# Kernel tuning notes

Hardware: AMD Instinct MI355X
Metric: run time of the kernel (lower is better)

The kernel has to match this reference:

```python
import jax, jax.numpy as jnp
import numpy as np

B, L, DM, H = 2, 4096, 1024, 16
D = DM // H


def setup_inputs() -> dict:
    key = jax.random.key(0)
    ks = jax.random.split(key, 11)
    s = 1.0 / np.sqrt(DM)
    return {
        "query": jax.random.normal(ks[0], (B, L, DM), jnp.float32),
        "key": jax.random.normal(ks[1], (B, L, DM), jnp.float32),
        "value": jax.random.normal(ks[2], (B, L, DM), jnp.float32),
        "Wq": jax.random.normal(ks[3], (DM, DM), jnp.float32) * s,
        "bq": jnp.zeros((DM,), jnp.float32),
        "Wk": jax.random.normal(ks[4], (DM, DM), jnp.float32) * s,
        "bk": jnp.zeros((DM,), jnp.float32),
        "Wv": jax.random.normal(ks[5], (DM, DM), jnp.float32) * s,
        "bv": jnp.zeros((DM,), jnp.float32),
        "Wo": jax.random.normal(ks[6], (DM, DM), jnp.float32) * s,
        "bo": jnp.zeros((DM,), jnp.float32),
    }


def _split_heads(x):
    # (B, L, DM) -> (B, H, L, D)
    b, l, _ = x.shape
    return x.reshape(b, l, H, D).transpose(0, 2, 1, 3)


def reference(query, key, value, Wq, bq, Wk, bk, Wv, bv, Wo, bo):
    q = _split_heads(query @ Wq + bq)
    k = _split_heads(key @ Wk + bk)
    v = _split_heads(value @ Wv + bv)
    # ELU+1 feature map
    q = jax.nn.elu(q) + 1.0
    k = jax.nn.elu(k) + 1.0
    # Original: kv = einsum('bhld,bhmd->bhlm', k, v); out = einsum('bhlm,bhld->bhmd', kv, q)
    # Equivalent (associativity): out[m,d] = sum_e v[m,e] * (sum_l k[l,e] q[l,d])
    S = jnp.einsum('bhle,bhld->bhed', k, q)          # (B,H,D,D)
    out = jnp.einsum('bhme,bhed->bhmd', v, S)        # (B,H,L,D)
    denom = jnp.einsum('bhld,bhld->bhl', q, k) + 1e-6
    out = out / denom[..., None]
    # combine heads: (B,H,L,D) -> (B,L,DM)
    out = out.transpose(0, 2, 1, 3).reshape(out.shape[0], -1, DM)
    # out_dense; dropout is identity at inference
    return out @ Wo + bo
```

## Files before the change

kernel.cpp:

```cpp
#include <hip/hip_runtime.h>

#define B_  2
#define L_  4096
#define DM_ 1024
#define H_  16
#define D_  64
#define M_  (B_ * L_)

typedef unsigned short u16;
typedef short bf16x8 __attribute__((ext_vector_type(8)));
typedef float f32x4  __attribute__((ext_vector_type(4)));

typedef const __attribute__((address_space(1))) void* as1_cvp;
typedef __attribute__((address_space(3))) void* as3_vp;

__device__ __forceinline__ float b2f(u16 u) {
    union { unsigned int i; float f; } x; x.i = ((unsigned int)u) << 16; return x.f;
}
__device__ __forceinline__ u16 f2b(float f) {
    unsigned int x = __float_as_uint(f);
    return (u16)((x + 0x7fffu + ((x >> 16) & 1u)) >> 16);
}

__global__ void prep_kernel(
    const float* __restrict__ query, const float* __restrict__ key, const float* __restrict__ value,
    u16* __restrict__ qb, u16* __restrict__ kb, u16* __restrict__ vb,
    const float* __restrict__ w0, const float* __restrict__ w1,
    const float* __restrict__ w2, const float* __restrict__ w3,
    u16* __restrict__ t0, u16* __restrict__ t1, u16* __restrict__ t2, u16* __restrict__ t3)
{
    __shared__ float tile[32][33];
    const int bx = blockIdx.x;
    const int t  = threadIdx.x;
    if (bx < 24576) {
        int z = bx >> 13;
        int i = (bx & 8191) * 256 + t;
        const float* in = z == 0 ? query : (z == 1 ? key : value);
        u16* out        = z == 0 ? qb    : (z == 1 ? kb  : vb);
        float4 v = ((const float4*)in)[i];
        ushort4 o;
        o.x = f2b(v.x); o.y = f2b(v.y); o.z = f2b(v.z); o.w = f2b(v.w);
        ((ushort4*)out)[i] = o;
    } else {
        int bz = bx - 24576;
        int z  = bz >> 10;
        int rem = bz & 1023;
        int gx = rem & 31, gy = rem >> 5;
        const float* W = z == 0 ? w0 : z == 1 ? w1 : z == 2 ? w2 : w3;
        u16* Wt        = z == 0 ? t0 : z == 1 ? t1 : z == 2 ? t2 : t3;
        int tx = t & 31, ty = t >> 5;
        int n  = gx * 32 + tx;
        int k0 = gy * 32;
#pragma unroll
        for (int i = 0; i < 4; ++i)
            tile[ty + i * 8][tx] = W[(size_t)(k0 + ty + i * 8) * DM_ + n];
        __syncthreads();
#pragma unroll
        for (int i = 0; i < 4; ++i) {
            int nn = gx * 32 + ty + i * 8;
            Wt[(size_t)nn * DM_ + k0 + tx] = f2b(tile[tx][ty + i * 8]);
        }
    }
}

__global__ __launch_bounds__(256, 4) void gemm_qkv_kernel(
    const u16* __restrict__ qb, const u16* __restrict__ kb, const u16* __restrict__ vb,
    const u16* __restrict__ Wqt, const u16* __restrict__ Wkt, const u16* __restrict__ Wvt,
    const float* __restrict__ bq, const float* __restrict__ bk, const float* __restrict__ bv,
    u16* __restrict__ QpT, u16* __restrict__ KpT, u16* __restrict__ Vp)
{
    const int z = blockIdx.z;
    const u16* A    = z == 0 ? qb  : z == 1 ? kb  : vb;
    const u16* Bt   = z == 0 ? Wqt : z == 1 ? Wkt : Wvt;
    const float* bias = z == 0 ? bq : z == 1 ? bk : bv;

    __shared__ __align__(16) u16 smem[16384];
    u16* As = smem;
    u16* Bs = smem + 8192;

    const int t    = threadIdx.x;
    const int lane = t & 63;
    const int wave = t >> 6;
    const int wr   = wave >> 1;
    const int wc   = wave & 1;
    const int quad = lane >> 4;
    const int l16  = lane & 15;
    const int m0   = blockIdx.x * 128;
    const int n0   = blockIdx.y * 128;
    const int K    = DM_;

    f32x4 acc[4][4] = {};

    for (int kt = 0; kt < K; kt += 64) {
#pragma unroll
        for (int i = 0; i < 4; ++i) {
            int c   = i * 256 + t;
            int row = c >> 3;
            int kc  = c & 7;
            int cbase = i * 256 + wave * 64;
            const u16* gA = A  + (size_t)(m0 + row) * K + kt + kc * 8;
            const u16* gB = Bt + (size_t)(n0 + row) * K + kt + kc * 8;
            __builtin_amdgcn_global_load_lds((as1_cvp)gA, (as3_vp)(As + cbase * 8), 16, 0, 0);
            __builtin_amdgcn_global_load_lds((as1_cvp)gB, (as3_vp)(Bs + cbase * 8), 16, 0, 0);
        }
        __syncthreads();
#pragma unroll
        for (int ks = 0; ks < 2; ++ks) {
            bf16x8 af[4], bfr[4];
#pragma unroll
            for (int it = 0; it < 4; ++it)
                af[it] = *(const bf16x8*)(As + (wr * 64 + it * 16 + l16) * 64 + ks * 32 + quad * 8);
#pragma unroll
            for (int jt = 0; jt < 4; ++jt)
                bfr[jt] = *(const bf16x8*)(Bs + (wc * 64 + jt * 16 + l16) * 64 + ks * 32 + quad * 8);
#pragma unroll
            for (int it = 0; it < 4; ++it)
#pragma unroll
                for (int jt = 0; jt < 4; ++jt)
                    acc[it][jt] = __builtin_amdgcn_mfma_f32_16x16x32_bf16(
                        af[it], bfr[jt], acc[it][jt], 0, 0, 0);
        }
        __syncthreads();
    }

    if (z == 2) {
#pragma unroll
        for (int it = 0; it < 4; ++it) {
            int row0 = m0 + wr * 64 + it * 16 + quad * 4;
#pragma unroll
            for (int jt = 0; jt < 4; ++jt) {
                int col = n0 + wc * 64 + jt * 16 + l16;
                float bv2 = bias[col];
#pragma unroll
                for (int r = 0; r < 4; ++r)
                    Vp[(size_t)(row0 + r) * DM_ + col] = f2b(acc[it][jt][r] + bv2);
            }
        }
    } else {
        u16* OutT = z == 0 ? QpT : KpT;
        u16* Ct = smem;
        __syncthreads();
#pragma unroll
        for (int it = 0; it < 4; ++it) {
            int row0 = wr * 64 + it * 16 + quad * 4;
#pragma unroll
            for (int jt = 0; jt < 4; ++jt) {
                int colr = wc * 64 + jt * 16 + l16;
                float bv2 = bias[n0 + colr];
                float x0 = acc[it][jt][0] + bv2;
                float x1 = acc[it][jt][1] + bv2;
                float x2 = acc[it][jt][2] + bv2;
                float x3 = acc[it][jt][3] + bv2;
                x0 = (x0 > 0.f) ? (x0 + 1.f) : __expf(x0);
                x1 = (x1 > 0.f) ? (x1 + 1.f) : __expf(x1);
                x2 = (x2 > 0.f) ? (x2 + 1.f) : __expf(x2);
                x3 = (x3 > 0.f) ? (x3 + 1.f) : __expf(x3);
                ushort4 o;
                o.x = f2b(x0); o.y = f2b(x1); o.z = f2b(x2); o.w = f2b(x3);
                *(ushort4*)&Ct[colr * 128 + row0] = o;
            }
        }
        __syncthreads();
        int b   = m0 >> 12;
        int seg = t & 15;
        int cg  = t >> 4;
#pragma unroll
        for (int iter = 0; iter < 8; ++iter) {
            int colIdx = iter * 16 + cg;
            int gcol = n0 + colIdx;
            int bh = b * 16 + (gcol >> 6);
            int e  = gcol & 63;
            uint4 v = *(const uint4*)&Ct[colIdx * 128 + seg * 8];
            *(uint4*)(OutT + ((size_t)bh << 18) + ((size_t)e << 12)
                      + (m0 & 4095) + seg * 8) = v;
        }
    }
}

__global__ __launch_bounds__(256, 5) void gemm_out_kernel(
    const u16* __restrict__ A, const u16* __restrict__ Bt,
    const float* __restrict__ bias, float* __restrict__ Cout)
{
    __shared__ __align__(16) u16 smem[12288];
    u16* As = smem;
    u16* Bs = smem + 4096;

    const int t    = threadIdx.x;
    const int lane = t & 63;
    const int wave = t >> 6;
    const int wr   = wave >> 1;
    const int wc   = wave & 1;
    const int quad = lane >> 4;
    const int l16  = lane & 15;
    const int m0   = blockIdx.x * 64;
    const int n0   = blockIdx.y * 128;
    const int K    = DM_;

    f32x4 acc[2][4] = {};

    for (int kt = 0; kt < K; kt += 64) {
#pragma unroll
        for (int i = 0; i < 2; ++i) {
            int c   = i * 256 + t;
            int row = c >> 3;
            int kc  = c & 7;
            int cbase = i * 256 + wave * 64;
            const u16* gA = A + (size_t)(m0 + row) * K + kt + kc * 8;
            __builtin_amdgcn_global_load_lds((as1_cvp)gA, (as3_vp)(As + cbase * 8), 16, 0, 0);
        }
#pragma unroll
        for (int i = 0; i < 4; ++i) {
            int c   = i * 256 + t;
            int row = c >> 3;
            int kc  = c & 7;
            int cbase = i * 256 + wave * 64;
            const u16* gB = Bt + (size_t)(n0 + row) * K + kt + kc * 8;
            __builtin_amdgcn_global_load_lds((as1_cvp)gB, (as3_vp)(Bs + cbase * 8), 16, 0, 0);
        }
        __syncthreads();
#pragma unroll
        for (int ks = 0; ks < 2; ++ks) {
            bf16x8 af[2], bfr[4];
#pragma unroll
            for (int it = 0; it < 2; ++it)
                af[it] = *(const bf16x8*)(As + (wr * 32 + it * 16 + l16) * 64 + ks * 32 + quad * 8);
#pragma unroll
            for (int jt = 0; jt < 4; ++jt)
                bfr[jt] = *(const bf16x8*)(Bs + (wc * 64 + jt * 16 + l16) * 64 + ks * 32 + quad * 8);
#pragma unroll
            for (int it = 0; it < 2; ++it)
#pragma unroll
                for (int jt = 0; jt < 4; ++jt)
                    acc[it][jt] = __builtin_amdgcn_mfma_f32_16x16x32_bf16(
                        af[it], bfr[jt], acc[it][jt], 0, 0, 0);
        }
        __syncthreads();
    }

#pragma unroll
    for (int it = 0; it < 2; ++it) {
        int row0 = m0 + wr * 32 + it * 16 + quad * 4;
#pragma unroll
        for (int jt = 0; jt < 4; ++jt) {
            int col = n0 + wc * 64 + jt * 16 + l16;
            float bv = bias[col];
#pragma unroll
            for (int r = 0; r < 4; ++r)
                Cout[(size_t)(row0 + r) * DM_ + col] = acc[it][jt][r] + bv;
        }
    }
}

__global__ __launch_bounds__(256) void attn_s_kernel(
    const u16* __restrict__ QpT, const u16* __restrict__ KpT,
    float* __restrict__ S_part, float* __restrict__ denom)
{
    const int t    = threadIdx.x;
    const int lane = t & 63;
    const int wave = t >> 6;
    const int quad = lane >> 4;
    const int l16  = lane & 15;
    const int bh   = blockIdx.x;
    const int lc   = blockIdx.y * 512;

    const u16* baseQ = QpT + ((size_t)bh << 18);
    const u16* baseK = KpT + ((size_t)bh << 18);

    f32x4 acc[4] = {};
    const u16* arow = baseK + (size_t)(wave * 16 + l16) * 4096 + lc;
#pragma unroll 4
    for (int ks = 0; ks < 16; ++ks) {
        int koff = ks * 32 + quad * 8;
        bf16x8 a = *(const bf16x8*)(arow + koff);
#pragma unroll
        for (int dt = 0; dt < 4; ++dt) {
            bf16x8 b = *(const bf16x8*)(baseQ + (size_t)(dt * 16 + l16) * 4096 + lc + koff);
            acc[dt] = __builtin_amdgcn_mfma_f32_16x16x32_bf16(a, b, acc[dt], 0, 0, 0);
        }
    }
    float* Sp = S_part + ((size_t)blockIdx.y * 32 + bh) * 4096;
#pragma unroll
    for (int dt = 0; dt < 4; ++dt)
#pragma unroll
        for (int r = 0; r < 4; ++r)
            Sp[(wave * 16 + quad * 4 + r) * 64 + dt * 16 + l16] = acc[dt][r];

    {
        float s0 = 0.f, s1 = 0.f;
        int off = lc + 2 * t;
#pragma unroll 8
        for (int e = 0; e < 64; ++e) {
            unsigned int qv = *(const unsigned int*)(baseQ + (size_t)e * 4096 + off);
            unsigned int kv = *(const unsigned int*)(baseK + (size_t)e * 4096 + off);
            s0 += b2f((u16)(qv & 0xffff)) * b2f((u16)(kv & 0xffff));
            s1 += b2f((u16)(qv >> 16))   * b2f((u16)(kv >> 16));
        }
        denom[(size_t)bh * 4096 + off]     = s0 + 1e-6f;
        denom[(size_t)bh * 4096 + off + 1] = s1 + 1e-6f;
    }
}

__global__ __launch_bounds__(256) void attn_out_kernel(
    const u16* __restrict__ Vp, const float* __restrict__ S_part,
    const float* __restrict__ denom, u16* __restrict__ ctx)
{
    __shared__ __align__(16) u16 Sb[64 * 64];
    __shared__ float dsh[256];
    const int t    = threadIdx.x;
    const int lane = t & 63;
    const int wave = t >> 6;
    const int quad = lane >> 4;
    const int l16  = lane & 15;
    const int bh   = blockIdx.x;
    const int b    = bh >> 4, h = bh & 15;
    const int lc   = blockIdx.y * 256;

    {
        const float* Sg = S_part + (size_t)bh * 4096;
        int e = t >> 2, d0 = (t & 3) * 16;
        float tmp[16];
#pragma unroll
        for (int i = 0; i < 16; ++i) tmp[i] = 0.f;
#pragma unroll
        for (int p = 0; p < 8; ++p) {
            const float* Sgp = Sg + (size_t)p * 32 * 4096;
#pragma unroll
            for (int i = 0; i < 16; ++i) tmp[i] += Sgp[e * 64 + d0 + i];
        }
#pragma unroll
        for (int i = 0; i < 16; ++i)
            Sb[(d0 + i) * 64 + e] = f2b(tmp[i]);
        dsh[t] = denom[(size_t)bh * 4096 + lc + t];
    }
    __syncthreads();

    const u16* Abase = Vp + (size_t)b * L_ * DM_ + (size_t)(lc + wave * 64 + l16) * DM_ + h * 64;
    f32x4 acc[4][4] = {};
#pragma unroll
    for (int ks = 0; ks < 2; ++ks) {
        int koff = ks * 32 + quad * 8;
        bf16x8 af[4], bfr[4];
#pragma unroll
        for (int lt = 0; lt < 4; ++lt)
            af[lt] = *(const bf16x8*)(Abase + (size_t)(lt * 16) * DM_ + koff);
#pragma unroll
        for (int dt = 0; dt < 4; ++dt)
            bfr[dt] = *(const bf16x8*)(Sb + (dt * 16 + l16) * 64 + koff);
#pragma unroll
        for (int lt = 0; lt < 4; ++lt)
#pragma unroll
            for (int dt = 0; dt < 4; ++dt)
                acc[lt][dt] = __builtin_amdgcn_mfma_f32_16x16x32_bf16(
                    af[lt], bfr[dt], acc[lt][dt], 0, 0, 0);
    }

    u16* cbase = ctx + (size_t)b * L_ * DM_ + h * 64;
#pragma unroll
    for (int lt = 0; lt < 4; ++lt) {
        int lrow0 = wave * 64 + lt * 16 + quad * 4;
        float inv[4];
#pragma unroll
        for (int r = 0; r < 4; ++r) inv[r] = 1.f / dsh[lrow0 + r];
#pragma unroll
        for (int dt = 0; dt < 4; ++dt) {
            int d = dt * 16 + l16;
#pragma unroll
            for (int r = 0; r < 4; ++r)
                cbase[(size_t)(lc + lrow0 + r) * DM_ + d] = f2b(acc[lt][dt][r] * inv[r]);
        }
    }
}

extern "C" void kernel_launch(void* const* d_in, const int* in_sizes, int n_in,
                              void* d_out, int out_size, void* d_ws, size_t ws_size,
                              hipStream_t stream)
{
    const float* query = (const float*)d_in[0];
    const float* key   = (const float*)d_in[1];
    const float* value = (const float*)d_in[2];
    const float* Wq = (const float*)d_in[3];  const float* bq = (const float*)d_in[4];
    const float* Wk = (const float*)d_in[5];  const float* bk = (const float*)d_in[6];
    const float* Wv = (const float*)d_in[7];  const float* bv = (const float*)d_in[8];
    const float* Wo = (const float*)d_in[9];  const float* bo = (const float*)d_in[10];

    const size_t SZ = (size_t)M_ * DM_ * sizeof(u16);
    char* ws = (char*)d_ws;
    u16* qb  = (u16*)(ws + 0 * SZ);
    u16* kb  = (u16*)(ws + 1 * SZ);
    u16* vb  = (u16*)(ws + 2 * SZ);
    u16* QpT = (u16*)(ws + 3 * SZ);
    u16* KpT = (u16*)(ws + 4 * SZ);
    u16* Vp  = (u16*)(ws + 5 * SZ);
    u16* ctx = (u16*)(ws + 6 * SZ);
    u16* Wqt = (u16*)(ws + 7 * SZ);
    u16* Wkt = Wqt + (size_t)DM_ * DM_;
    u16* Wvt = Wkt + (size_t)DM_ * DM_;
    u16* Wot = Wvt + (size_t)DM_ * DM_;
    float* S_part = (float*)(ws + 7 * SZ + 4 * (size_t)DM_ * DM_ * sizeof(u16));
    float* denom  = S_part + (size_t)8 * 32 * 4096;

    prep_kernel<<<28672, 256, 0, stream>>>(
        query, key, value, qb, kb, vb, Wq, Wk, Wv, Wo, Wqt, Wkt, Wvt, Wot);

    gemm_qkv_kernel<<<dim3(M_ / 128, DM_ / 128, 3), 256, 0, stream>>>(
        qb, kb, vb, Wqt, Wkt, Wvt, bq, bk, bv, QpT, KpT, Vp);

    attn_s_kernel<<<dim3(B_ * H_, L_ / 512), 256, 0, stream>>>(QpT, KpT, S_part, denom);

    attn_out_kernel<<<dim3(B_ * H_, L_ / 256), 256, 0, stream>>>(Vp, S_part, denom, ctx);

    gemm_out_kernel<<<dim3(M_ / 64, DM_ / 128), 256, 0, stream>>>(
        ctx, Wot, bo, (float*)d_out);
}
```

Before: 287.7 us.

## Swizzle LDS tiles, pad transpose buffer, and coarsen prep and attn_s work

Applies an XOR swizzle to the LDS layouts in both GEMMs and in the S tile of attn_out, so the MFMA operand reads avoid bank conflicts. It also pads the transpose staging buffer and drops a redundant barrier. The prep kernel now converts two float4 per thread, and attn_s processes 1024 rows per block with wider denominator loads, which halves the partial-S count reduced in attn_out. The coarsening reduces grid size and parallelism in attn_s in exchange for less reduction and launch overhead.

```diff
diff --git a/kernel.cpp b/kernel.cpp
--- a/kernel.cpp
+++ b/kernel.cpp
@@ -32,17 +32,20 @@
     __shared__ float tile[32][33];
     const int bx = blockIdx.x;
     const int t  = threadIdx.x;
-    if (bx < 24576) {
-        int z = bx >> 13;
-        int i = (bx & 8191) * 256 + t;
+    if (bx < 12288) {
+        int z = bx >> 12;
+        int i = (bx & 4095) * 256 + t;
         const float* in = z == 0 ? query : (z == 1 ? key : value);
         u16* out        = z == 0 ? qb    : (z == 1 ? kb  : vb);
-        float4 v = ((const float4*)in)[i];
-        ushort4 o;
-        o.x = f2b(v.x); o.y = f2b(v.y); o.z = f2b(v.z); o.w = f2b(v.w);
-        ((ushort4*)out)[i] = o;
+        float4 v0 = ((const float4*)in)[2 * i];
+        float4 v1 = ((const float4*)in)[2 * i + 1];
+        ushort4 o0, o1;
+        o0.x = f2b(v0.x); o0.y = f2b(v0.y); o0.z = f2b(v0.z); o0.w = f2b(v0.w);
+        o1.x = f2b(v1.x); o1.y = f2b(v1.y); o1.z = f2b(v1.z); o1.w = f2b(v1.w);
+        ((ushort4*)out)[2 * i]     = o0;
+        ((ushort4*)out)[2 * i + 1] = o1;
     } else {
-        int bz = bx - 24576;
+        int bz = bx - 12288;
         int z  = bz >> 10;
         int rem = bz & 1023;
         int gx = rem & 31, gy = rem >> 5;
@@ -74,7 +77,7 @@
     const u16* Bt   = z == 0 ? Wqt : z == 1 ? Wkt : Wvt;
     const float* bias = z == 0 ? bq : z == 1 ? bk : bv;
 
-    __shared__ __align__(16) u16 smem[16384];
+    __shared__ __align__(16) u16 smem[17408];
     u16* As = smem;
     u16* Bs = smem + 8192;
 
@@ -85,6 +88,7 @@
     const int wc   = wave & 1;
     const int quad = lane >> 4;
     const int l16  = lane & 15;
+    const int swz  = l16 & 7;
     const int m0   = blockIdx.x * 128;
     const int n0   = blockIdx.y * 128;
     const int K    = DM_;
@@ -96,7 +100,7 @@
         for (int i = 0; i < 4; ++i) {
             int c   = i * 256 + t;
             int row = c >> 3;
-            int kc  = c & 7;
+            int kc  = (c & 7) ^ (row & 7);
             int cbase = i * 256 + wave * 64;
             const u16* gA = A  + (size_t)(m0 + row) * K + kt + kc * 8;
             const u16* gB = Bt + (size_t)(n0 + row) * K + kt + kc * 8;
@@ -106,13 +110,14 @@
         __syncthreads();
 #pragma unroll
         for (int ks = 0; ks < 2; ++ks) {
+            int skc = (ks * 4 + quad) ^ swz;
             bf16x8 af[4], bfr[4];
 #pragma unroll
             for (int it = 0; it < 4; ++it)
-                af[it] = *(const bf16x8*)(As + (wr * 64 + it * 16 + l16) * 64 + ks * 32 + quad * 8);
+                af[it] = *(const bf16x8*)(As + (wr * 64 + it * 16 + l16) * 64 + skc * 8);
 #pragma unroll
             for (int jt = 0; jt < 4; ++jt)
-                bfr[jt] = *(const bf16x8*)(Bs + (wc * 64 + jt * 16 + l16) * 64 + ks * 32 + quad * 8);
+                bfr[jt] = *(const bf16x8*)(Bs + (wc * 64 + jt * 16 + l16) * 64 + skc * 8);
 #pragma unroll
             for (int it = 0; it < 4; ++it)
 #pragma unroll
@@ -139,7 +144,6 @@
     } else {
         u16* OutT = z == 0 ? QpT : KpT;
         u16* Ct = smem;
-        __syncthreads();
 #pragma unroll
         for (int it = 0; it < 4; ++it) {
             int row0 = wr * 64 + it * 16 + quad * 4;
@@ -157,7 +161,7 @@
                 x3 = (x3 > 0.f) ? (x3 + 1.f) : __expf(x3);
                 ushort4 o;
                 o.x = f2b(x0); o.y = f2b(x1); o.z = f2b(x2); o.w = f2b(x3);
-                *(ushort4*)&Ct[colr * 128 + row0] = o;
+                *(ushort4*)&Ct[colr * 136 + row0] = o;
             }
         }
         __syncthreads();
@@ -170,7 +174,7 @@
             int gcol = n0 + colIdx;
             int bh = b * 16 + (gcol >> 6);
             int e  = gcol & 63;
-            uint4 v = *(const uint4*)&Ct[colIdx * 128 + seg * 8];
+            uint4 v = *(const uint4*)&Ct[colIdx * 136 + seg * 8];
             *(uint4*)(OutT + ((size_t)bh << 18) + ((size_t)e << 12)
                       + (m0 & 4095) + seg * 8) = v;
         }
@@ -192,6 +196,7 @@
     const int wc   = wave & 1;
     const int quad = lane >> 4;
     const int l16  = lane & 15;
+    const int swz  = l16 & 7;
     const int m0   = blockIdx.x * 64;
     const int n0   = blockIdx.y * 128;
     const int K    = DM_;
@@ -203,7 +208,7 @@
         for (int i = 0; i < 2; ++i) {
             int c   = i * 256 + t;
             int row = c >> 3;
-            int kc  = c & 7;
+            int kc  = (c & 7) ^ (row & 7);
             int cbase = i * 256 + wave * 64;
             const u16* gA = A + (size_t)(m0 + row) * K + kt + kc * 8;
             __builtin_amdgcn_global_load_lds((as1_cvp)gA, (as3_vp)(As + cbase * 8), 16, 0, 0);
@@ -212,7 +217,7 @@
         for (int i = 0; i < 4; ++i) {
             int c   = i * 256 + t;
             int row = c >> 3;
-            int kc  = c & 7;
+            int kc  = (c & 7) ^ (row & 7);
             int cbase = i * 256 + wave * 64;
             const u16* gB = Bt + (size_t)(n0 + row) * K + kt + kc * 8;
             __builtin_amdgcn_global_load_lds((as1_cvp)gB, (as3_vp)(Bs + cbase * 8), 16, 0, 0);
@@ -220,13 +225,14 @@
         __syncthreads();
 #pragma unroll
         for (int ks = 0; ks < 2; ++ks) {
+            int skc = (ks * 4 + quad) ^ swz;
             bf16x8 af[2], bfr[4];
 #pragma unroll
             for (int it = 0; it < 2; ++it)
-                af[it] = *(const bf16x8*)(As + (wr * 32 + it * 16 + l16) * 64 + ks * 32 + quad * 8);
+                af[it] = *(const bf16x8*)(As + (wr * 32 + it * 16 + l16) * 64 + skc * 8);
 #pragma unroll
             for (int jt = 0; jt < 4; ++jt)
-                bfr[jt] = *(const bf16x8*)(Bs + (wc * 64 + jt * 16 + l16) * 64 + ks * 32 + quad * 8);
+                bfr[jt] = *(const bf16x8*)(Bs + (wc * 64 + jt * 16 + l16) * 64 + skc * 8);
 #pragma unroll
             for (int it = 0; it < 2; ++it)
 #pragma unroll
@@ -261,7 +267,7 @@
     const int quad = lane >> 4;
     const int l16  = lane & 15;
     const int bh   = blockIdx.x;
-    const int lc   = blockIdx.y * 512;
+    const int lc   = blockIdx.y * 1024;
 
     const u16* baseQ = QpT + ((size_t)bh << 18);
     const u16* baseK = KpT + ((size_t)bh << 18);
@@ -269,7 +275,7 @@
     f32x4 acc[4] = {};
     const u16* arow = baseK + (size_t)(wave * 16 + l16) * 4096 + lc;
 #pragma unroll 4
-    for (int ks = 0; ks < 16; ++ks) {
+    for (int ks = 0; ks < 32; ++ks) {
         int koff = ks * 32 + quad * 8;
         bf16x8 a = *(const bf16x8*)(arow + koff);
 #pragma unroll
@@ -286,17 +292,20 @@
             Sp[(wave * 16 + quad * 4 + r) * 64 + dt * 16 + l16] = acc[dt][r];
 
     {
-        float s0 = 0.f, s1 = 0.f;
-        int off = lc + 2 * t;
+        float s0 = 0.f, s1 = 0.f, s2 = 0.f, s3 = 0.f;
+        int off = lc + 4 * t;
 #pragma unroll 8
         for (int e = 0; e < 64; ++e) {
-            unsigned int qv = *(const unsigned int*)(baseQ + (size_t)e * 4096 + off);
-            unsigned int kv = *(const unsigned int*)(baseK + (size_t)e * 4096 + off);
-            s0 += b2f((u16)(qv & 0xffff)) * b2f((u16)(kv & 0xffff));
-            s1 += b2f((u16)(qv >> 16))   * b2f((u16)(kv >> 16));
-        }
-        denom[(size_t)bh * 4096 + off]     = s0 + 1e-6f;
-        denom[(size_t)bh * 4096 + off + 1] = s1 + 1e-6f;
+            uint2 qv = *(const uint2*)(baseQ + (size_t)e * 4096 + off);
+            uint2 kv = *(const uint2*)(baseK + (size_t)e * 4096 + off);
+            s0 += b2f((u16)(qv.x & 0xffff)) * b2f((u16)(kv.x & 0xffff));
+            s1 += b2f((u16)(qv.x >> 16))   * b2f((u16)(kv.x >> 16));
+            s2 += b2f((u16)(qv.y & 0xffff)) * b2f((u16)(kv.y & 0xffff));
+            s3 += b2f((u16)(qv.y >> 16))   * b2f((u16)(kv.y >> 16));
+        }
+        float* dp = denom + (size_t)bh * 4096 + off;
+        dp[0] = s0 + 1e-6f; dp[1] = s1 + 1e-6f;
+        dp[2] = s2 + 1e-6f; dp[3] = s3 + 1e-6f;
     }
 }
 
@@ -322,14 +331,17 @@
 #pragma unroll
         for (int i = 0; i < 16; ++i) tmp[i] = 0.f;
 #pragma unroll
-        for (int p = 0; p < 8; ++p) {
+        for (int p = 0; p < 4; ++p) {
             const float* Sgp = Sg + (size_t)p * 32 * 4096;
 #pragma unroll
             for (int i = 0; i < 16; ++i) tmp[i] += Sgp[e * 64 + d0 + i];
         }
-#pragma unroll
-        for (int i = 0; i < 16; ++i)
-            Sb[(d0 + i) * 64 + e] = f2b(tmp[i]);
+        int ec = e >> 3, el = e & 7;
+#pragma unroll
+        for (int i = 0; i < 16; ++i) {
+            int d = d0 + i;
+            Sb[d * 64 + ((ec ^ (d & 7)) << 3) + el] = f2b(tmp[i]);
+        }
         dsh[t] = denom[(size_t)bh * 4096 + lc + t];
     }
     __syncthreads();
@@ -339,13 +351,16 @@
 #pragma unroll
     for (int ks = 0; ks < 2; ++ks) {
         int koff = ks * 32 + quad * 8;
+        int kc   = ks * 4 + quad;
         bf16x8 af[4], bfr[4];
 #pragma unroll
         for (int lt = 0; lt < 4; ++lt)
             af[lt] = *(const bf16x8*)(Abase + (size_t)(lt * 16) * DM_ + koff);
 #pragma unroll
-        for (int dt = 0; dt < 4; ++dt)
-            bfr[dt] = *(const bf16x8*)(Sb + (dt * 16 + l16) * 64 + koff);
+        for (int dt = 0; dt < 4; ++dt) {
+            int d = dt * 16 + l16;
+            bfr[dt] = *(const bf16x8*)(Sb + d * 64 + ((kc ^ (d & 7)) << 3));
+        }
 #pragma unroll
         for (int lt = 0; lt < 4; ++lt)
 #pragma unroll
@@ -397,15 +412,15 @@
     u16* Wvt = Wkt + (size_t)DM_ * DM_;
     u16* Wot = Wvt + (size_t)DM_ * DM_;
     float* S_part = (float*)(ws + 7 * SZ + 4 * (size_t)DM_ * DM_ * sizeof(u16));
-    float* denom  = S_part + (size_t)8 * 32 * 4096;
-
-    prep_kernel<<<28672, 256, 0, stream>>>(
+    float* denom  = S_part + (size_t)4 * 32 * 4096;
+
+    prep_kernel<<<16384, 256, 0, stream>>>(
         query, key, value, qb, kb, vb, Wq, Wk, Wv, Wo, Wqt, Wkt, Wvt, Wot);
 
     gemm_qkv_kernel<<<dim3(M_ / 128, DM_ / 128, 3), 256, 0, stream>>>(
         qb, kb, vb, Wqt, Wkt, Wvt, bq, bk, bv, QpT, KpT, Vp);
 
-    attn_s_kernel<<<dim3(B_ * H_, L_ / 512), 256, 0, stream>>>(QpT, KpT, S_part, denom);
+    attn_s_kernel<<<dim3(B_ * H_, L_ / 1024), 256, 0, stream>>>(QpT, KpT, S_part, denom);
 
     attn_out_kernel<<<dim3(B_ * H_, L_ / 256), 256, 0, stream>>>(Vp, S_part, denom, ctx);
 
```

Result: no change. 284.2 us (-1.2%).
